# Performance work log

Hardware: AMD Instinct MI355X
Metric: run time of the kernel (lower is better)

Reference implementation:

```python
import jax, jax.numpy as jnp
import numpy as np
import math

TAU = 0.5        # module stores self.tau = 1.0 / tau with tau=2.0
THRESHOLD = 1.0
SURR_C = 1.0 / (2.0 * math.sqrt(2.0 * math.pi))  # coefficient in Stochastic.backward


@jax.custom_vjp
def spike(v):
    # Stochastic.forward: (input > 0).float()
    return (v > 0).astype(v.dtype)


def _spike_fwd(v):
    return spike(v), v


def _spike_bwd(v, g):
    # Stochastic.backward: grad * 1/(2*sqrt(2*pi)) * exp(-v^2/2)
    return (g * (SURR_C * jnp.exp(-0.5 * v * v)),)


spike.defvjp(_spike_fwd, _spike_bwd)


def setup_inputs() -> dict:
    key = jax.random.key(0)
    x = jax.random.normal(key, (32, 128, 8192), dtype=jnp.float32)  # [B, T, N]
    return {"x": x}


def reference(x):
    # Eval-mode iterative stochastic-LIF update (no noise injection).
    xt = jnp.swapaxes(x, 0, 1)  # [T, B, N] for scan over time

    def step(u, x_t):
        u = TAU * u + x_t                # leaky integrate
        o = spike(u - THRESHOLD)         # fire
        u = u * (1.0 - o)                # hard reset by multiply
        return u, o

    u0 = jnp.zeros_like(xt[0])
    _, o = jax.lax.scan(step, u0, xt)
    return jnp.swapaxes(o, 0, 1)  # [B, T, N]
```

## Files before the change

### kernel.cpp

```cpp
#include <hip/hip_runtime.h>


constexpr int B  = 32;
constexpr int T  = 128;
constexpr int N  = 8192;
constexpr int N4 = N / 4;

__global__ __launch_bounds__(256) void lif_kernel(const float4* __restrict__ x,
                                                  float4* __restrict__ out) {
    int idx = blockIdx.x * blockDim.x + threadIdx.x;
    int b = idx >> 11;
    int n = idx & (N4 - 1);
    size_t base = (size_t)b * T * N4 + n;
    const float4* xp = x   + base;
    float4*       op = out + base;

    float ux = 0.f, uy = 0.f, uz = 0.f, uw = 0.f;
    #pragma unroll 8
    for (int t = 0; t < T; ++t) {
        float4 xt = xp[(size_t)t * N4];
        float4 o;
        ux = 0.5f * ux + xt.x;  o.x = (ux > 1.0f) ? 1.0f : 0.0f;  ux = (ux > 1.0f) ? 0.0f : ux;
        uy = 0.5f * uy + xt.y;  o.y = (uy > 1.0f) ? 1.0f : 0.0f;  uy = (uy > 1.0f) ? 0.0f : uy;
        uz = 0.5f * uz + xt.z;  o.z = (uz > 1.0f) ? 1.0f : 0.0f;  uz = (uz > 1.0f) ? 0.0f : uz;
        uw = 0.5f * uw + xt.w;  o.w = (uw > 1.0f) ? 1.0f : 0.0f;  uw = (uw > 1.0f) ? 0.0f : uw;
        op[(size_t)t * N4] = o;
    }
}

extern "C" void kernel_launch(void* const* d_in, const int* in_sizes, int n_in,
                              void* d_out, int out_size, void* d_ws, size_t ws_size,
                              hipStream_t stream) {
    const float4* x  = (const float4*)d_in[0];
    float4*      out = (float4*)d_out;
    int total = B * N4;
    lif_kernel<<<total / 256, 256, 0, stream>>>(x, out);
}
```

Before: 237.7 us.

## Split time axis into chunks with warm-up recurrence for more parallelism

```diff
diff --git a/kernel.cpp b/kernel.cpp
--- a/kernel.cpp
+++ b/kernel.cpp
@@ -5,26 +5,65 @@
 constexpr int T  = 128;
 constexpr int N  = 8192;
 constexpr int N4 = N / 4;
+constexpr int C  = 4;
+constexpr int L  = 32;
+constexpr int W  = 32;
+
+__device__ __forceinline__ void warm4(float4& u, const float4 xt) {
+    u.x = 0.5f * u.x + xt.x;  u.x = (u.x > 1.0f) ? 0.0f : u.x;
+    u.y = 0.5f * u.y + xt.y;  u.y = (u.y > 1.0f) ? 0.0f : u.y;
+    u.z = 0.5f * u.z + xt.z;  u.z = (u.z > 1.0f) ? 0.0f : u.z;
+    u.w = 0.5f * u.w + xt.w;  u.w = (u.w > 1.0f) ? 0.0f : u.w;
+}
+
+__device__ __forceinline__ void step4(float4& u, const float4 xt, float4& o) {
+    u.x = 0.5f * u.x + xt.x;  o.x = (u.x > 1.0f) ? 1.0f : 0.0f;  u.x = (u.x > 1.0f) ? 0.0f : u.x;
+    u.y = 0.5f * u.y + xt.y;  o.y = (u.y > 1.0f) ? 1.0f : 0.0f;  u.y = (u.y > 1.0f) ? 0.0f : u.y;
+    u.z = 0.5f * u.z + xt.z;  o.z = (u.z > 1.0f) ? 1.0f : 0.0f;  u.z = (u.z > 1.0f) ? 0.0f : u.z;
+    u.w = 0.5f * u.w + xt.w;  o.w = (u.w > 1.0f) ? 1.0f : 0.0f;  u.w = (u.w > 1.0f) ? 0.0f : u.w;
+}
 
 __global__ __launch_bounds__(256) void lif_kernel(const float4* __restrict__ x,
                                                   float4* __restrict__ out) {
     int idx = blockIdx.x * blockDim.x + threadIdx.x;
-    int b = idx >> 11;
-    int n = idx & (N4 - 1);
+    int c   = idx >> 16;
+    int rem = idx & 65535;
+    int b   = rem >> 11;
+    int n   = rem & (N4 - 1);
     size_t base = (size_t)b * T * N4 + n;
     const float4* xp = x   + base;
     float4*       op = out + base;
 
-    float ux = 0.f, uy = 0.f, uz = 0.f, uw = 0.f;
-    #pragma unroll 8
-    for (int t = 0; t < T; ++t) {
-        float4 xt = xp[(size_t)t * N4];
-        float4 o;
-        ux = 0.5f * ux + xt.x;  o.x = (ux > 1.0f) ? 1.0f : 0.0f;  ux = (ux > 1.0f) ? 0.0f : ux;
-        uy = 0.5f * uy + xt.y;  o.y = (uy > 1.0f) ? 1.0f : 0.0f;  uy = (uy > 1.0f) ? 0.0f : uy;
-        uz = 0.5f * uz + xt.z;  o.z = (uz > 1.0f) ? 1.0f : 0.0f;  uz = (uz > 1.0f) ? 0.0f : uz;
-        uw = 0.5f * uw + xt.w;  o.w = (uw > 1.0f) ? 1.0f : 0.0f;  uw = (uw > 1.0f) ? 0.0f : uw;
-        op[(size_t)t * N4] = o;
+    const int t0 = c * L;
+    float4 u = make_float4(0.f, 0.f, 0.f, 0.f);
+
+    if (c > 0) {
+        const int tw = t0 - W;
+        #pragma unroll
+        for (int blk = 0; blk < W / 8; ++blk) {
+            float4 xs[8];
+            #pragma unroll
+            for (int j = 0; j < 8; ++j)
+                xs[j] = xp[(size_t)(tw + blk * 8 + j) * N4];
+            #pragma unroll
+            for (int j = 0; j < 8; ++j)
+                warm4(u, xs[j]);
+        }
+    }
+
+    #pragma unroll
+    for (int blk = 0; blk < L / 8; ++blk) {
+        float4 xs[8];
+        #pragma unroll
+        for (int j = 0; j < 8; ++j)
+            xs[j] = xp[(size_t)(t0 + blk * 8 + j) * N4];
+        float4 os[8];
+        #pragma unroll
+        for (int j = 0; j < 8; ++j)
+            step4(u, xs[j], os[j]);
+        #pragma unroll
+        for (int j = 0; j < 8; ++j)
+            op[(size_t)(t0 + blk * 8 + j) * N4] = os[j];
     }
 }
 
@@ -33,6 +72,6 @@
                               hipStream_t stream) {
     const float4* x  = (const float4*)d_in[0];
     float4*      out = (float4*)d_out;
-    int total = B * N4;
+    int total = B * N4 * C;
     lif_kernel<<<total / 256, 256, 0, stream>>>(x, out);
 }
```

After: 238.6 us. No clear change (+0.4%).
